# Performance work log

Measured on AMD Instinct MI355X. Metric: run time of the kernel, lower is better.

The kernel has to match this reference:

```python
import jax, jax.numpy as jnp
import numpy as np

NUM_USERS = 100000
NUM_ITEMS = 50000
EMBED_DIM = 64
N_LAYERS = 3
N_EDGES = 2400000
N_NODES = NUM_USERS + NUM_ITEMS


def setup_inputs() -> dict:
    key = jax.random.key(0)
    k1, k2, k3 = jax.random.split(key, 3)
    # Xavier-uniform init for embedding tables
    bound_u = float(np.sqrt(6.0 / (NUM_USERS + EMBED_DIM)))
    bound_i = float(np.sqrt(6.0 / (NUM_ITEMS + EMBED_DIM)))
    user_emb = jax.random.uniform(k1, (NUM_USERS, EMBED_DIM), jnp.float32, -bound_u, bound_u)
    item_emb = jax.random.uniform(k2, (NUM_ITEMS, EMBED_DIM), jnp.float32, -bound_i, bound_i)
    edge_index = jax.random.randint(k3, (2, N_EDGES), 0, N_NODES, dtype=jnp.int32)
    return {"user_emb": user_emb, "item_emb": item_emb, "edge_index": edge_index}


def _propagate(x, row, col):
    # degree-normalized gather-scale-scatter: out[row] += x[col] * rsqrt(deg[row]*deg[col])
    n = x.shape[0]
    deg = jnp.clip(jnp.zeros((n,), x.dtype).at[row].add(1.0), 1.0)  # bincount, clamp(min=1)
    norm = jax.lax.rsqrt(deg[row]) * jax.lax.rsqrt(deg[col])        # [E]
    return jnp.zeros_like(x).at[row].add(x[col] * norm[:, None])   # scatter-add [N,d]


def reference(user_emb, item_emb, edge_index):
    row, col = edge_index[0], edge_index[1]
    all_emb = jnp.concatenate([user_emb, item_emb], axis=0)  # [N, d]
    acc = all_emb
    x = all_emb
    for _ in range(N_LAYERS):
        x = _propagate(x, row, col)
        acc = acc + x
    final_emb = acc / (N_LAYERS + 1)  # mean over layer-0..n_layers embeddings
    return final_emb[:NUM_USERS], final_emb[NUM_USERS:]
```

## Files before the change

kernel.cpp:

```cpp
#include <hip/hip_runtime.h>


#define NUM_USERS 100000
#define NUM_ITEMS 50000
#define EMBED_DIM 64
#define N_NODES   150000
#define N_EDGES   2400000
#define N_BUCKETS 586
#define BCAP      4608
#define PART_BLOCKS 256

#define OFF_BCNT 0
#define OFF_BE   8192
#define OFF_RSQD 1208192
#define OFF_PS   1808256
#define OFF_XA   12611584
#define OFF_XB   31813632

__device__ __forceinline__ unsigned f2bf(float f) {
    unsigned u = __float_as_uint(f);
    return (u + 0x7fffu + ((u >> 16) & 1u)) >> 16;
}
__device__ __forceinline__ float bflo(unsigned u) { return __uint_as_float(u << 16); }
__device__ __forceinline__ float bfhi(unsigned u) { return __uint_as_float(u & 0xffff0000u); }
__device__ __forceinline__ float2 bf2(unsigned u) {
    float2 r; r.x = bflo(u); r.y = bfhi(u); return r;
}

__global__ void partition_kernel(const int4* __restrict__ row4, const int4* __restrict__ col4,
                                 int* __restrict__ bcnt, unsigned* __restrict__ ps,
                                 uint2* __restrict__ yA, uint2* __restrict__ yB) {
    __shared__ int lh[N_BUCKETS];
    if (blockIdx.x == 0 && threadIdx.x < 16) {
        uint2 z; z.x = 0u; z.y = 0u;
        yA[2400000 + threadIdx.x] = z;
        yB[2400000 + threadIdx.x] = z;
    }
    for (int t = threadIdx.x; t < N_BUCKETS; t += blockDim.x) lh[t] = 0;
    __syncthreads();
    const int total4 = N_EDGES / 4;
    int per4 = (total4 + gridDim.x - 1) / gridDim.x;
    int s4 = blockIdx.x * per4;
    int e4 = s4 + per4; if (e4 > total4) e4 = total4;
    for (int i = s4 + (int)threadIdx.x; i < e4; i += (int)blockDim.x) {
        int4 r = row4[i];
        atomicAdd(&lh[r.x >> 8], 1);
        atomicAdd(&lh[r.y >> 8], 1);
        atomicAdd(&lh[r.z >> 8], 1);
        atomicAdd(&lh[r.w >> 8], 1);
    }
    __syncthreads();
    for (int t = threadIdx.x; t < N_BUCKETS; t += blockDim.x) {
        int c = lh[t];
        lh[t] = c ? (t * BCAP + atomicAdd(&bcnt[t], c)) : 0;
    }
    __syncthreads();
    for (int i = s4 + (int)threadIdx.x; i < e4; i += (int)blockDim.x) {
        int4 r = row4[i];
        int4 c = col4[i];
        int pos;
        pos = atomicAdd(&lh[r.x >> 8], 1); ps[pos] = ((unsigned)(r.x & 255) << 18) | (unsigned)c.x;
        pos = atomicAdd(&lh[r.y >> 8], 1); ps[pos] = ((unsigned)(r.y & 255) << 18) | (unsigned)c.y;
        pos = atomicAdd(&lh[r.z >> 8], 1); ps[pos] = ((unsigned)(r.z & 255) << 18) | (unsigned)c.z;
        pos = atomicAdd(&lh[r.w >> 8], 1); ps[pos] = ((unsigned)(r.w & 255) << 18) | (unsigned)c.w;
    }
}

__global__ void fine_kernel(const int* __restrict__ bcnt, int* __restrict__ ps,
                            int2* __restrict__ be, float* __restrict__ rsqd,
                            const float4* __restrict__ user, const float4* __restrict__ item,
                            uint2* __restrict__ yA) {
    __shared__ int ledge[BCAP];
    __shared__ int rh[256];
    __shared__ int rsc[256];
    __shared__ int rcur[256];
    __shared__ float rq[256];
    int b = blockIdx.x;
    int base = b * BCAP;
    int cnt  = bcnt[b];
    if (cnt > BCAP) cnt = BCAP;
    rh[threadIdx.x] = 0;
    __syncthreads();
    for (int i = threadIdx.x; i < cnt; i += 256) {
        int p = ps[base + i];
        ledge[i] = p;
        atomicAdd(&rh[p >> 18], 1);
    }
    __syncthreads();
    rsc[threadIdx.x] = (rh[threadIdx.x] + 1) & ~1;
    __syncthreads();
    for (int off = 1; off < 256; off <<= 1) {
        int t = (threadIdx.x >= off) ? rsc[threadIdx.x - off] : 0;
        __syncthreads();
        rsc[threadIdx.x] += t;
        __syncthreads();
    }
    {
        int r = threadIdx.x;
        int sz = (rh[r] + 1) & ~1;
        int pstart = rsc[r] - sz;
        rcur[r] = pstart;
        int n = (b << 8) + r;
        if (n < N_NODES) {
            int2 p; p.x = base + pstart; p.y = base + pstart + rh[r];
            be[n] = p;
            float d = (float)(rh[r] < 1 ? 1 : rh[r]);
            float rn = rsqrtf(d);
            rq[r] = rn;
            rsqd[n] = rn;
        }
    }
    __syncthreads();
    for (int i = threadIdx.x; i < cnt; i += 256) {
        int p = ledge[i];
        int pos = atomicAdd(&rcur[p >> 18], 1);
        ps[base + pos] = p & 0x3FFFF;
    }
    for (int idx = threadIdx.x; idx < 4096; idx += 256) {
        int r = idx >> 4, w = idx & 15;
        int n = (b << 8) + r;
        if (n < N_NODES) {
            const float4* src = (n < NUM_USERS) ? (user + (size_t)n * 16)
                                                : (item + (size_t)(n - NUM_USERS) * 16);
            float4 v = src[w];
            float rn = rq[r];
            uint2 o;
            o.x = f2bf(v.x * rn) | (f2bf(v.y * rn) << 16);
            o.y = f2bf(v.z * rn) | (f2bf(v.w * rn) << 16);
            yA[(size_t)n * 16 + w] = o;
        }
    }
}

__device__ __forceinline__ void pull_sum(int n, int q, const int2* __restrict__ be,
                                         const int2* __restrict__ scol2,
                                         const uint4* __restrict__ xin, float2 sum[4]) {
    int2 bnd = be[n];
    int endj = bnd.y;
    for (int j = bnd.x; j < endj; j += 8) {
        int h = j >> 1;
        int2 cc0 = scol2[h];
        int2 cc1 = scol2[h + 1];
        int2 cc2 = scol2[h + 2];
        int2 cc3 = scol2[h + 3];
        int c0 = cc0.x;
        int c1 = (j + 1 < endj) ? cc0.y : N_NODES;
        int c2 = (j + 2 < endj) ? cc1.x : N_NODES;
        int c3 = (j + 3 < endj) ? cc1.y : N_NODES;
        int c4 = (j + 4 < endj) ? cc2.x : N_NODES;
        int c5 = (j + 5 < endj) ? cc2.y : N_NODES;
        int c6 = (j + 6 < endj) ? cc3.x : N_NODES;
        int c7 = (j + 7 < endj) ? cc3.y : N_NODES;
        uint4 X0 = xin[(size_t)c0 * 8 + q];
        uint4 X1 = xin[(size_t)c1 * 8 + q];
        uint4 X2 = xin[(size_t)c2 * 8 + q];
        uint4 X3 = xin[(size_t)c3 * 8 + q];
        uint4 X4 = xin[(size_t)c4 * 8 + q];
        uint4 X5 = xin[(size_t)c5 * 8 + q];
        uint4 X6 = xin[(size_t)c6 * 8 + q];
        uint4 X7 = xin[(size_t)c7 * 8 + q];
        sum[0] += (bf2(X0.x) + bf2(X1.x)) + (bf2(X2.x) + bf2(X3.x))
                + (bf2(X4.x) + bf2(X5.x)) + (bf2(X6.x) + bf2(X7.x));
        sum[1] += (bf2(X0.y) + bf2(X1.y)) + (bf2(X2.y) + bf2(X3.y))
                + (bf2(X4.y) + bf2(X5.y)) + (bf2(X6.y) + bf2(X7.y));
        sum[2] += (bf2(X0.z) + bf2(X1.z)) + (bf2(X2.z) + bf2(X3.z))
                + (bf2(X4.z) + bf2(X5.z)) + (bf2(X6.z) + bf2(X7.z));
        sum[3] += (bf2(X0.w) + bf2(X1.w)) + (bf2(X2.w) + bf2(X3.w))
                + (bf2(X4.w) + bf2(X5.w)) + (bf2(X6.w) + bf2(X7.w));
    }
}

__global__ void pull_kernel(const int2* __restrict__ be,
                            const int2* __restrict__ scol2, const float* __restrict__ rsqd,
                            const uint4* __restrict__ xin, uint4* __restrict__ xout) {
    int t = blockIdx.x * blockDim.x + (int)threadIdx.x;
    int n = t >> 3;
    if (n >= N_NODES) return;
    int q = t & 7;
    float rn = rsqd[n];
    float2 sum[4];
    sum[0] = make_float2(0.f, 0.f); sum[1] = make_float2(0.f, 0.f);
    sum[2] = make_float2(0.f, 0.f); sum[3] = make_float2(0.f, 0.f);
    pull_sum(n, q, be, scol2, xin, sum);
    float s2 = rn * rn;
    uint4 p;
    p.x = f2bf(sum[0].x * s2) | (f2bf(sum[0].y * s2) << 16);
    p.y = f2bf(sum[1].x * s2) | (f2bf(sum[1].y * s2) << 16);
    p.z = f2bf(sum[2].x * s2) | (f2bf(sum[2].y * s2) << 16);
    p.w = f2bf(sum[3].x * s2) | (f2bf(sum[3].y * s2) << 16);
    xout[(size_t)n * 8 + q] = p;
}

__global__ void pull_last_kernel(const int2* __restrict__ be,
                                 const int2* __restrict__ scol2, const float* __restrict__ rsqd,
                                 const uint4* __restrict__ xin,
                                 const uint4* __restrict__ xprev,
                                 const float4* __restrict__ user, const float4* __restrict__ item,
                                 float4* __restrict__ acc4) {
    int t = blockIdx.x * blockDim.x + (int)threadIdx.x;
    int n = t >> 3;
    if (n >= N_NODES) return;
    int q = t & 7;
    float rn = rsqd[n];
    float2 sum[4];
    sum[0] = make_float2(0.f, 0.f); sum[1] = make_float2(0.f, 0.f);
    sum[2] = make_float2(0.f, 0.f); sum[3] = make_float2(0.f, 0.f);
    pull_sum(n, q, be, scol2, xin, sum);
    float sd = 1.0f / rn;
    uint4 p2 = xin  [(size_t)n * 8 + q];
    uint4 p1 = xprev[(size_t)n * 8 + q];
    const float4* x0 = (n < NUM_USERS) ? (user + (size_t)n * 16)
                                       : (item + (size_t)(n - NUM_USERS) * 16);
    float4 a0 = x0[q * 2], a1 = x0[q * 2 + 1];
    float4 o0, o1;
    o0.x = (a0.x + (bflo(p1.x) + bflo(p2.x)) * sd + rn * sum[0].x) * 0.25f;
    o0.y = (a0.y + (bfhi(p1.x) + bfhi(p2.x)) * sd + rn * sum[0].y) * 0.25f;
    o0.z = (a0.z + (bflo(p1.y) + bflo(p2.y)) * sd + rn * sum[1].x) * 0.25f;
    o0.w = (a0.w + (bfhi(p1.y) + bfhi(p2.y)) * sd + rn * sum[1].y) * 0.25f;
    o1.x = (a1.x + (bflo(p1.z) + bflo(p2.z)) * sd + rn * sum[2].x) * 0.25f;
    o1.y = (a1.y + (bfhi(p1.z) + bfhi(p2.z)) * sd + rn * sum[2].y) * 0.25f;
    o1.z = (a1.z + (bflo(p1.w) + bflo(p2.w)) * sd + rn * sum[3].x) * 0.25f;
    o1.w = (a1.w + (bfhi(p1.w) + bfhi(p2.w)) * sd + rn * sum[3].y) * 0.25f;
    size_t o4 = (size_t)n * 16 + q * 2;
    acc4[o4] = o0;
    acc4[o4 + 1] = o1;
}

extern "C" void kernel_launch(void* const* d_in, const int* in_sizes, int n_in,
                              void* d_out, int out_size, void* d_ws, size_t ws_size,
                              hipStream_t stream) {
    const float* user = (const float*)d_in[0];
    const float* item = (const float*)d_in[1];
    const int*   ei   = (const int*)d_in[2];
    const int* row = ei;
    const int* col = ei + N_EDGES;

    char*  ws   = (char*)d_ws;
    int*   bcnt = (int*)(ws + OFF_BCNT);
    int2*  be   = (int2*)(ws + OFF_BE);
    float* rsqd = (float*)(ws + OFF_RSQD);
    int*   ps   = (int*)(ws + OFF_PS);
    char*  xA   = ws + OFF_XA;
    char*  xB   = ws + OFF_XB;
    float* acc  = (float*)d_out;

    hipMemsetAsync(bcnt, 0, N_BUCKETS * sizeof(int), stream);
    partition_kernel<<<PART_BLOCKS, 1024, 0, stream>>>((const int4*)row, (const int4*)col,
                                                       bcnt, (unsigned*)ps,
                                                       (uint2*)xA, (uint2*)xB);
    fine_kernel<<<N_BUCKETS, 256, 0, stream>>>(bcnt, ps, be, rsqd,
                                               (const float4*)user, (const float4*)item,
                                               (uint2*)xA);

    const int grid = (N_NODES * 8 + 255) / 256;
    pull_kernel<<<grid, 256, 0, stream>>>(be, (const int2*)ps, rsqd,
        (const uint4*)xA, (uint4*)xB);
    pull_kernel<<<grid, 256, 0, stream>>>(be, (const int2*)ps, rsqd,
        (const uint4*)xB, (uint4*)xA);
    pull_last_kernel<<<grid, 256, 0, stream>>>(be, (const int2*)ps, rsqd,
        (const uint4*)xA, (const uint4*)xB,
        (const float4*)user, (const float4*)item, (float4*)acc);
}
```

Baseline: 284.6 us.

## Sort nodes by degree into a permutation to balance pull-kernel wavefronts

Adds a degree histogram in fine_kernel and a new dperm_kernel that buckets nodes by in-degree into a permutation array. The pull kernels then process nodes in degree-sorted order, so lanes in a wavefront have similar loop trip counts and divergence drops. The rsqrt-degree array is dropped and recomputed from the edge bounds. fine_kernel now runs with 512 threads. The cost is an extra kernel launch, an extra indirection per node, and scattered output writes and self-row reads that lose locality.

New measurement: 694.3 us. 2.44x slower.

```diff
diff --git a/kernel.cpp b/kernel.cpp
--- a/kernel.cpp
+++ b/kernel.cpp
@@ -10,12 +10,14 @@
 #define BCAP      4608
 #define PART_BLOCKS 256
 
-#define OFF_BCNT 0
-#define OFF_BE   8192
-#define OFF_RSQD 1208192
-#define OFF_PS   1808256
-#define OFF_XA   12611584
-#define OFF_XB   31813632
+#define OFF_BCNT  0
+#define OFF_DBINS 4096
+#define OFF_DCUR  4352
+#define OFF_BE    8192
+#define OFF_PERM  1208192
+#define OFF_PS    1808256
+#define OFF_XA    12611584
+#define OFF_XB    31813632
 
 __device__ __forceinline__ unsigned f2bf(float f) {
     unsigned u = __float_as_uint(f);
@@ -67,7 +69,7 @@
 }
 
 __global__ void fine_kernel(const int* __restrict__ bcnt, int* __restrict__ ps,
-                            int2* __restrict__ be, float* __restrict__ rsqd,
+                            int2* __restrict__ be, int* __restrict__ dbins,
                             const float4* __restrict__ user, const float4* __restrict__ item,
                             uint2* __restrict__ yA) {
     __shared__ int ledge[BCAP];
@@ -75,27 +77,29 @@
     __shared__ int rsc[256];
     __shared__ int rcur[256];
     __shared__ float rq[256];
+    __shared__ int dh[64];
     int b = blockIdx.x;
     int base = b * BCAP;
     int cnt  = bcnt[b];
     if (cnt > BCAP) cnt = BCAP;
-    rh[threadIdx.x] = 0;
-    __syncthreads();
-    for (int i = threadIdx.x; i < cnt; i += 256) {
+    if (threadIdx.x < 256) rh[threadIdx.x] = 0;
+    if (threadIdx.x < 64) dh[threadIdx.x] = 0;
+    __syncthreads();
+    for (int i = threadIdx.x; i < cnt; i += blockDim.x) {
         int p = ps[base + i];
         ledge[i] = p;
         atomicAdd(&rh[p >> 18], 1);
     }
     __syncthreads();
-    rsc[threadIdx.x] = (rh[threadIdx.x] + 1) & ~1;
+    if (threadIdx.x < 256) rsc[threadIdx.x] = (rh[threadIdx.x] + 1) & ~1;
     __syncthreads();
     for (int off = 1; off < 256; off <<= 1) {
-        int t = (threadIdx.x >= off) ? rsc[threadIdx.x - off] : 0;
+        int t = (threadIdx.x < 256 && threadIdx.x >= off) ? rsc[threadIdx.x - off] : 0;
         __syncthreads();
-        rsc[threadIdx.x] += t;
+        if (threadIdx.x < 256) rsc[threadIdx.x] += t;
         __syncthreads();
     }
-    {
+    if (threadIdx.x < 256) {
         int r = threadIdx.x;
         int sz = (rh[r] + 1) & ~1;
         int pstart = rsc[r] - sz;
@@ -105,18 +109,22 @@
             int2 p; p.x = base + pstart; p.y = base + pstart + rh[r];
             be[n] = p;
             float d = (float)(rh[r] < 1 ? 1 : rh[r]);
-            float rn = rsqrtf(d);
-            rq[r] = rn;
-            rsqd[n] = rn;
+            rq[r] = rsqrtf(d);
+            int bin = rh[r] < 63 ? rh[r] : 63;
+            atomicAdd(&dh[bin], 1);
         }
     }
     __syncthreads();
-    for (int i = threadIdx.x; i < cnt; i += 256) {
+    if (threadIdx.x < 64) {
+        int v = dh[threadIdx.x];
+        if (v) atomicAdd(&dbins[threadIdx.x], v);
+    }
+    for (int i = threadIdx.x; i < cnt; i += blockDim.x) {
         int p = ledge[i];
         int pos = atomicAdd(&rcur[p >> 18], 1);
         ps[base + pos] = p & 0x3FFFF;
     }
-    for (int idx = threadIdx.x; idx < 4096; idx += 256) {
+    for (int idx = threadIdx.x; idx < 4096; idx += blockDim.x) {
         int r = idx >> 4, w = idx & 15;
         int n = (b << 8) + r;
         if (n < N_NODES) {
@@ -132,10 +140,31 @@
     }
 }
 
-__device__ __forceinline__ void pull_sum(int n, int q, const int2* __restrict__ be,
+__global__ void dperm_kernel(const int2* __restrict__ be, const int* __restrict__ dbins,
+                             int* __restrict__ dcur, int* __restrict__ perm) {
+    __shared__ int binv[64];
+    __shared__ int base[64];
+    if (threadIdx.x < 64) binv[threadIdx.x] = dbins[threadIdx.x];
+    __syncthreads();
+    if (threadIdx.x < 64) {
+        int s = 0;
+        for (int bb = 0; bb < (int)threadIdx.x; ++bb) s += binv[bb];
+        base[threadIdx.x] = s;
+    }
+    __syncthreads();
+    for (int n = blockIdx.x * blockDim.x + (int)threadIdx.x; n < N_NODES;
+         n += gridDim.x * blockDim.x) {
+        int2 p = be[n];
+        int deg = p.y - p.x;
+        int bin = deg < 63 ? deg : 63;
+        int slot = base[bin] + atomicAdd(&dcur[bin], 1);
+        perm[slot] = n;
+    }
+}
+
+__device__ __forceinline__ void pull_sum(int2 bnd, int q,
                                          const int2* __restrict__ scol2,
                                          const uint4* __restrict__ xin, float2 sum[4]) {
-    int2 bnd = be[n];
     int endj = bnd.y;
     for (int j = bnd.x; j < endj; j += 8) {
         int h = j >> 1;
@@ -170,29 +199,33 @@
     }
 }
 
-__global__ void pull_kernel(const int2* __restrict__ be,
-                            const int2* __restrict__ scol2, const float* __restrict__ rsqd,
+__global__ void pull_kernel(const int* __restrict__ perm, const int2* __restrict__ be,
+                            const int2* __restrict__ scol2,
                             const uint4* __restrict__ xin, uint4* __restrict__ xout) {
     int t = blockIdx.x * blockDim.x + (int)threadIdx.x;
     int n = t >> 3;
     if (n >= N_NODES) return;
+    int pn = perm[n];
     int q = t & 7;
-    float rn = rsqd[n];
+    int2 bnd = be[pn];
     float2 sum[4];
     sum[0] = make_float2(0.f, 0.f); sum[1] = make_float2(0.f, 0.f);
     sum[2] = make_float2(0.f, 0.f); sum[3] = make_float2(0.f, 0.f);
-    pull_sum(n, q, be, scol2, xin, sum);
+    pull_sum(bnd, q, scol2, xin, sum);
+    int deg = bnd.y - bnd.x;
+    float d = (float)(deg < 1 ? 1 : deg);
+    float rn = rsqrtf(d);
     float s2 = rn * rn;
     uint4 p;
     p.x = f2bf(sum[0].x * s2) | (f2bf(sum[0].y * s2) << 16);
     p.y = f2bf(sum[1].x * s2) | (f2bf(sum[1].y * s2) << 16);
     p.z = f2bf(sum[2].x * s2) | (f2bf(sum[2].y * s2) << 16);
     p.w = f2bf(sum[3].x * s2) | (f2bf(sum[3].y * s2) << 16);
-    xout[(size_t)n * 8 + q] = p;
-}
-
-__global__ void pull_last_kernel(const int2* __restrict__ be,
-                                 const int2* __restrict__ scol2, const float* __restrict__ rsqd,
+    xout[(size_t)pn * 8 + q] = p;
+}
+
+__global__ void pull_last_kernel(const int* __restrict__ perm, const int2* __restrict__ be,
+                                 const int2* __restrict__ scol2,
                                  const uint4* __restrict__ xin,
                                  const uint4* __restrict__ xprev,
                                  const float4* __restrict__ user, const float4* __restrict__ item,
@@ -200,17 +233,21 @@
     int t = blockIdx.x * blockDim.x + (int)threadIdx.x;
     int n = t >> 3;
     if (n >= N_NODES) return;
+    int pn = perm[n];
     int q = t & 7;
-    float rn = rsqd[n];
+    int2 bnd = be[pn];
     float2 sum[4];
     sum[0] = make_float2(0.f, 0.f); sum[1] = make_float2(0.f, 0.f);
     sum[2] = make_float2(0.f, 0.f); sum[3] = make_float2(0.f, 0.f);
-    pull_sum(n, q, be, scol2, xin, sum);
-    float sd = 1.0f / rn;
-    uint4 p2 = xin  [(size_t)n * 8 + q];
-    uint4 p1 = xprev[(size_t)n * 8 + q];
-    const float4* x0 = (n < NUM_USERS) ? (user + (size_t)n * 16)
-                                       : (item + (size_t)(n - NUM_USERS) * 16);
+    pull_sum(bnd, q, scol2, xin, sum);
+    int deg = bnd.y - bnd.x;
+    float d = (float)(deg < 1 ? 1 : deg);
+    float rn = rsqrtf(d);
+    float sd = sqrtf(d);
+    uint4 p2 = xin  [(size_t)pn * 8 + q];
+    uint4 p1 = xprev[(size_t)pn * 8 + q];
+    const float4* x0 = (pn < NUM_USERS) ? (user + (size_t)pn * 16)
+                                        : (item + (size_t)(pn - NUM_USERS) * 16);
     float4 a0 = x0[q * 2], a1 = x0[q * 2 + 1];
     float4 o0, o1;
     o0.x = (a0.x + (bflo(p1.x) + bflo(p2.x)) * sd + rn * sum[0].x) * 0.25f;
@@ -221,7 +258,7 @@
     o1.y = (a1.y + (bfhi(p1.z) + bfhi(p2.z)) * sd + rn * sum[2].y) * 0.25f;
     o1.z = (a1.z + (bflo(p1.w) + bflo(p2.w)) * sd + rn * sum[3].x) * 0.25f;
     o1.w = (a1.w + (bfhi(p1.w) + bfhi(p2.w)) * sd + rn * sum[3].y) * 0.25f;
-    size_t o4 = (size_t)n * 16 + q * 2;
+    size_t o4 = (size_t)pn * 16 + q * 2;
     acc4[o4] = o0;
     acc4[o4 + 1] = o1;
 }
@@ -235,29 +272,32 @@
     const int* row = ei;
     const int* col = ei + N_EDGES;
 
-    char*  ws   = (char*)d_ws;
-    int*   bcnt = (int*)(ws + OFF_BCNT);
-    int2*  be   = (int2*)(ws + OFF_BE);
-    float* rsqd = (float*)(ws + OFF_RSQD);
-    int*   ps   = (int*)(ws + OFF_PS);
-    char*  xA   = ws + OFF_XA;
-    char*  xB   = ws + OFF_XB;
-    float* acc  = (float*)d_out;
-
-    hipMemsetAsync(bcnt, 0, N_BUCKETS * sizeof(int), stream);
+    char*  ws    = (char*)d_ws;
+    int*   bcnt  = (int*)(ws + OFF_BCNT);
+    int*   dbins = (int*)(ws + OFF_DBINS);
+    int*   dcur  = (int*)(ws + OFF_DCUR);
+    int2*  be    = (int2*)(ws + OFF_BE);
+    int*   perm  = (int*)(ws + OFF_PERM);
+    int*   ps    = (int*)(ws + OFF_PS);
+    char*  xA    = ws + OFF_XA;
+    char*  xB    = ws + OFF_XB;
+    float* acc   = (float*)d_out;
+
+    hipMemsetAsync(ws, 0, 8192, stream);
     partition_kernel<<<PART_BLOCKS, 1024, 0, stream>>>((const int4*)row, (const int4*)col,
                                                        bcnt, (unsigned*)ps,
                                                        (uint2*)xA, (uint2*)xB);
-    fine_kernel<<<N_BUCKETS, 256, 0, stream>>>(bcnt, ps, be, rsqd,
+    fine_kernel<<<N_BUCKETS, 512, 0, stream>>>(bcnt, ps, be, dbins,
                                                (const float4*)user, (const float4*)item,
                                                (uint2*)xA);
+    dperm_kernel<<<256, 256, 0, stream>>>(be, dbins, dcur, perm);
 
     const int grid = (N_NODES * 8 + 255) / 256;
-    pull_kernel<<<grid, 256, 0, stream>>>(be, (const int2*)ps, rsqd,
+    pull_kernel<<<grid, 256, 0, stream>>>(perm, be, (const int2*)ps,
         (const uint4*)xA, (uint4*)xB);
-    pull_kernel<<<grid, 256, 0, stream>>>(be, (const int2*)ps, rsqd,
+    pull_kernel<<<grid, 256, 0, stream>>>(perm, be, (const int2*)ps,
         (const uint4*)xB, (uint4*)xA);
-    pull_last_kernel<<<grid, 256, 0, stream>>>(be, (const int2*)ps, rsqd,
+    pull_last_kernel<<<grid, 256, 0, stream>>>(perm, be, (const int2*)ps,
         (const uint4*)xA, (const uint4*)xB,
         (const float4*)user, (const float4*)item, (float4*)acc);
 }
```

## Stage partitioned edges in LDS for coalesced writes; derive degree from bounds

Applied to the files above, without the earlier changes.

The partition kernel now scans per-block bucket counts, stages each bucket's edges contiguously in shared memory, and then writes them to global memory in contiguous runs, replacing scattered per-edge global writes. The rsqd array is removed, and the pull kernels recompute rsqrt/sqrt of the degree from the row bounds. The fine kernel is also launched with 512 threads. The aim is to cut scattered write traffic and one global read per node, at the cost of a binary search per staged edge and a large shared-memory footprint that may lower occupancy.

New measurement: 276.4 us. 2.9% less time.

```diff
diff --git a/kernel.cpp b/kernel.cpp
--- a/kernel.cpp
+++ b/kernel.cpp
@@ -9,13 +9,13 @@
 #define N_BUCKETS 586
 #define BCAP      4608
 #define PART_BLOCKS 256
-
-#define OFF_BCNT 0
-#define OFF_BE   8192
-#define OFF_RSQD 1208192
-#define OFF_PS   1808256
-#define OFF_XA   12611584
-#define OFF_XB   31813632
+#define MAX_BLK_EDGES 9376
+
+#define OFF_BCNT  0
+#define OFF_BE    8192
+#define OFF_PS    1808256
+#define OFF_XA    12611584
+#define OFF_XB    31813632
 
 __device__ __forceinline__ unsigned f2bf(float f) {
     unsigned u = __float_as_uint(f);
@@ -30,44 +30,73 @@
 __global__ void partition_kernel(const int4* __restrict__ row4, const int4* __restrict__ col4,
                                  int* __restrict__ bcnt, unsigned* __restrict__ ps,
                                  uint2* __restrict__ yA, uint2* __restrict__ yB) {
-    __shared__ int lh[N_BUCKETS];
+    __shared__ int scanws[1024];
+    __shared__ int lsize[N_BUCKETS];
+    __shared__ int lstart[N_BUCKETS + 1];
+    __shared__ int gbase[N_BUCKETS];
+    __shared__ int lcur[N_BUCKETS];
+    __shared__ unsigned staged[MAX_BLK_EDGES];
     if (blockIdx.x == 0 && threadIdx.x < 16) {
         uint2 z; z.x = 0u; z.y = 0u;
         yA[2400000 + threadIdx.x] = z;
         yB[2400000 + threadIdx.x] = z;
     }
-    for (int t = threadIdx.x; t < N_BUCKETS; t += blockDim.x) lh[t] = 0;
+    scanws[threadIdx.x] = 0;
     __syncthreads();
     const int total4 = N_EDGES / 4;
     int per4 = (total4 + gridDim.x - 1) / gridDim.x;
     int s4 = blockIdx.x * per4;
     int e4 = s4 + per4; if (e4 > total4) e4 = total4;
+    const int cntE = (e4 - s4) * 4;
     for (int i = s4 + (int)threadIdx.x; i < e4; i += (int)blockDim.x) {
         int4 r = row4[i];
-        atomicAdd(&lh[r.x >> 8], 1);
-        atomicAdd(&lh[r.y >> 8], 1);
-        atomicAdd(&lh[r.z >> 8], 1);
-        atomicAdd(&lh[r.w >> 8], 1);
-    }
-    __syncthreads();
-    for (int t = threadIdx.x; t < N_BUCKETS; t += blockDim.x) {
-        int c = lh[t];
-        lh[t] = c ? (t * BCAP + atomicAdd(&bcnt[t], c)) : 0;
-    }
+        atomicAdd(&scanws[r.x >> 8], 1);
+        atomicAdd(&scanws[r.y >> 8], 1);
+        atomicAdd(&scanws[r.z >> 8], 1);
+        atomicAdd(&scanws[r.w >> 8], 1);
+    }
+    __syncthreads();
+    int myv = scanws[threadIdx.x];
+    if (threadIdx.x < N_BUCKETS) lsize[threadIdx.x] = myv;
+    __syncthreads();
+    for (int off = 1; off < 1024; off <<= 1) {
+        int t = (threadIdx.x >= off) ? scanws[threadIdx.x - off] : 0;
+        __syncthreads();
+        scanws[threadIdx.x] += t;
+        __syncthreads();
+    }
+    if (threadIdx.x < N_BUCKETS) {
+        int incl = scanws[threadIdx.x];
+        int st = incl - lsize[threadIdx.x];
+        lstart[threadIdx.x] = st;
+        lcur[threadIdx.x] = st;
+        int c = lsize[threadIdx.x];
+        gbase[threadIdx.x] = c ? (threadIdx.x * BCAP + atomicAdd(&bcnt[threadIdx.x], c)) : 0;
+    }
+    if (threadIdx.x == 0) lstart[N_BUCKETS] = cntE;
     __syncthreads();
     for (int i = s4 + (int)threadIdx.x; i < e4; i += (int)blockDim.x) {
         int4 r = row4[i];
         int4 c = col4[i];
         int pos;
-        pos = atomicAdd(&lh[r.x >> 8], 1); ps[pos] = ((unsigned)(r.x & 255) << 18) | (unsigned)c.x;
-        pos = atomicAdd(&lh[r.y >> 8], 1); ps[pos] = ((unsigned)(r.y & 255) << 18) | (unsigned)c.y;
-        pos = atomicAdd(&lh[r.z >> 8], 1); ps[pos] = ((unsigned)(r.z & 255) << 18) | (unsigned)c.z;
-        pos = atomicAdd(&lh[r.w >> 8], 1); ps[pos] = ((unsigned)(r.w & 255) << 18) | (unsigned)c.w;
+        pos = atomicAdd(&lcur[r.x >> 8], 1); staged[pos] = ((unsigned)(r.x & 255) << 18) | (unsigned)c.x;
+        pos = atomicAdd(&lcur[r.y >> 8], 1); staged[pos] = ((unsigned)(r.y & 255) << 18) | (unsigned)c.y;
+        pos = atomicAdd(&lcur[r.z >> 8], 1); staged[pos] = ((unsigned)(r.z & 255) << 18) | (unsigned)c.z;
+        pos = atomicAdd(&lcur[r.w >> 8], 1); staged[pos] = ((unsigned)(r.w & 255) << 18) | (unsigned)c.w;
+    }
+    __syncthreads();
+    for (int i = (int)threadIdx.x; i < cntE; i += (int)blockDim.x) {
+        int lo = 0, hi = N_BUCKETS - 1;
+        while (lo < hi) {
+            int mid = (lo + hi + 1) >> 1;
+            if (lstart[mid] <= i) lo = mid; else hi = mid - 1;
+        }
+        ps[gbase[lo] + (i - lstart[lo])] = staged[i];
     }
 }
 
 __global__ void fine_kernel(const int* __restrict__ bcnt, int* __restrict__ ps,
-                            int2* __restrict__ be, float* __restrict__ rsqd,
+                            int2* __restrict__ be,
                             const float4* __restrict__ user, const float4* __restrict__ item,
                             uint2* __restrict__ yA) {
     __shared__ int ledge[BCAP];
@@ -79,23 +108,23 @@
     int base = b * BCAP;
     int cnt  = bcnt[b];
     if (cnt > BCAP) cnt = BCAP;
-    rh[threadIdx.x] = 0;
-    __syncthreads();
-    for (int i = threadIdx.x; i < cnt; i += 256) {
+    if (threadIdx.x < 256) rh[threadIdx.x] = 0;
+    __syncthreads();
+    for (int i = threadIdx.x; i < cnt; i += blockDim.x) {
         int p = ps[base + i];
         ledge[i] = p;
         atomicAdd(&rh[p >> 18], 1);
     }
     __syncthreads();
-    rsc[threadIdx.x] = (rh[threadIdx.x] + 1) & ~1;
+    if (threadIdx.x < 256) rsc[threadIdx.x] = (rh[threadIdx.x] + 1) & ~1;
     __syncthreads();
     for (int off = 1; off < 256; off <<= 1) {
-        int t = (threadIdx.x >= off) ? rsc[threadIdx.x - off] : 0;
-        __syncthreads();
-        rsc[threadIdx.x] += t;
-        __syncthreads();
-    }
-    {
+        int t = (threadIdx.x < 256 && threadIdx.x >= off) ? rsc[threadIdx.x - off] : 0;
+        __syncthreads();
+        if (threadIdx.x < 256) rsc[threadIdx.x] += t;
+        __syncthreads();
+    }
+    if (threadIdx.x < 256) {
         int r = threadIdx.x;
         int sz = (rh[r] + 1) & ~1;
         int pstart = rsc[r] - sz;
@@ -105,18 +134,16 @@
             int2 p; p.x = base + pstart; p.y = base + pstart + rh[r];
             be[n] = p;
             float d = (float)(rh[r] < 1 ? 1 : rh[r]);
-            float rn = rsqrtf(d);
-            rq[r] = rn;
-            rsqd[n] = rn;
+            rq[r] = rsqrtf(d);
         }
     }
     __syncthreads();
-    for (int i = threadIdx.x; i < cnt; i += 256) {
+    for (int i = threadIdx.x; i < cnt; i += blockDim.x) {
         int p = ledge[i];
         int pos = atomicAdd(&rcur[p >> 18], 1);
         ps[base + pos] = p & 0x3FFFF;
     }
-    for (int idx = threadIdx.x; idx < 4096; idx += 256) {
+    for (int idx = threadIdx.x; idx < 4096; idx += blockDim.x) {
         int r = idx >> 4, w = idx & 15;
         int n = (b << 8) + r;
         if (n < N_NODES) {
@@ -132,10 +159,9 @@
     }
 }
 
-__device__ __forceinline__ void pull_sum(int n, int q, const int2* __restrict__ be,
+__device__ __forceinline__ void pull_sum(int2 bnd, int q,
                                          const int2* __restrict__ scol2,
                                          const uint4* __restrict__ xin, float2 sum[4]) {
-    int2 bnd = be[n];
     int endj = bnd.y;
     for (int j = bnd.x; j < endj; j += 8) {
         int h = j >> 1;
@@ -171,17 +197,20 @@
 }
 
 __global__ void pull_kernel(const int2* __restrict__ be,
-                            const int2* __restrict__ scol2, const float* __restrict__ rsqd,
+                            const int2* __restrict__ scol2,
                             const uint4* __restrict__ xin, uint4* __restrict__ xout) {
     int t = blockIdx.x * blockDim.x + (int)threadIdx.x;
     int n = t >> 3;
     if (n >= N_NODES) return;
     int q = t & 7;
-    float rn = rsqd[n];
+    int2 bnd = be[n];
     float2 sum[4];
     sum[0] = make_float2(0.f, 0.f); sum[1] = make_float2(0.f, 0.f);
     sum[2] = make_float2(0.f, 0.f); sum[3] = make_float2(0.f, 0.f);
-    pull_sum(n, q, be, scol2, xin, sum);
+    pull_sum(bnd, q, scol2, xin, sum);
+    int deg = bnd.y - bnd.x;
+    float d = (float)(deg < 1 ? 1 : deg);
+    float rn = rsqrtf(d);
     float s2 = rn * rn;
     uint4 p;
     p.x = f2bf(sum[0].x * s2) | (f2bf(sum[0].y * s2) << 16);
@@ -192,7 +221,7 @@
 }
 
 __global__ void pull_last_kernel(const int2* __restrict__ be,
-                                 const int2* __restrict__ scol2, const float* __restrict__ rsqd,
+                                 const int2* __restrict__ scol2,
                                  const uint4* __restrict__ xin,
                                  const uint4* __restrict__ xprev,
                                  const float4* __restrict__ user, const float4* __restrict__ item,
@@ -201,12 +230,15 @@
     int n = t >> 3;
     if (n >= N_NODES) return;
     int q = t & 7;
-    float rn = rsqd[n];
+    int2 bnd = be[n];
     float2 sum[4];
     sum[0] = make_float2(0.f, 0.f); sum[1] = make_float2(0.f, 0.f);
     sum[2] = make_float2(0.f, 0.f); sum[3] = make_float2(0.f, 0.f);
-    pull_sum(n, q, be, scol2, xin, sum);
-    float sd = 1.0f / rn;
+    pull_sum(bnd, q, scol2, xin, sum);
+    int deg = bnd.y - bnd.x;
+    float d = (float)(deg < 1 ? 1 : deg);
+    float rn = rsqrtf(d);
+    float sd = sqrtf(d);
     uint4 p2 = xin  [(size_t)n * 8 + q];
     uint4 p1 = xprev[(size_t)n * 8 + q];
     const float4* x0 = (n < NUM_USERS) ? (user + (size_t)n * 16)
@@ -238,26 +270,25 @@
     char*  ws   = (char*)d_ws;
     int*   bcnt = (int*)(ws + OFF_BCNT);
     int2*  be   = (int2*)(ws + OFF_BE);
-    float* rsqd = (float*)(ws + OFF_RSQD);
     int*   ps   = (int*)(ws + OFF_PS);
     char*  xA   = ws + OFF_XA;
     char*  xB   = ws + OFF_XB;
     float* acc  = (float*)d_out;
 
-    hipMemsetAsync(bcnt, 0, N_BUCKETS * sizeof(int), stream);
+    hipMemsetAsync(bcnt, 0, 4096, stream);
     partition_kernel<<<PART_BLOCKS, 1024, 0, stream>>>((const int4*)row, (const int4*)col,
                                                        bcnt, (unsigned*)ps,
                                                        (uint2*)xA, (uint2*)xB);
-    fine_kernel<<<N_BUCKETS, 256, 0, stream>>>(bcnt, ps, be, rsqd,
+    fine_kernel<<<N_BUCKETS, 512, 0, stream>>>(bcnt, ps, be,
                                                (const float4*)user, (const float4*)item,
                                                (uint2*)xA);
 
     const int grid = (N_NODES * 8 + 255) / 256;
-    pull_kernel<<<grid, 256, 0, stream>>>(be, (const int2*)ps, rsqd,
+    pull_kernel<<<grid, 256, 0, stream>>>(be, (const int2*)ps,
         (const uint4*)xA, (uint4*)xB);
-    pull_kernel<<<grid, 256, 0, stream>>>(be, (const int2*)ps, rsqd,
+    pull_kernel<<<grid, 256, 0, stream>>>(be, (const int2*)ps,
         (const uint4*)xB, (uint4*)xA);
-    pull_last_kernel<<<grid, 256, 0, stream>>>(be, (const int2*)ps, rsqd,
+    pull_last_kernel<<<grid, 256, 0, stream>>>(be, (const int2*)ps,
         (const uint4*)xA, (const uint4*)xB,
         (const float4*)user, (const float4*)item, (float4*)acc);
 }
```
